# Kernel optimization log

Hardware: AMD Instinct MI355X
Metric: run time of the kernel (lower is better)

## Reference

```python
import jax, jax.numpy as jnp
import numpy as np

EPS = 1e-08


def setup_inputs() -> dict:
    key = jax.random.key(0)
    k1, k2, k3 = jax.random.split(key, 3)
    N = 4000000
    x = jax.random.normal(k1, (N, 3), dtype=jnp.float32)
    x_gt = jax.random.normal(k2, (N, 3), dtype=jnp.float32)
    weights = jax.random.uniform(k3, (N,), dtype=jnp.float32)
    return {"x": x, "x_gt": x_gt, "weights": weights}


def reference(x, x_gt, weights):
    # weights: [N] -> [N, 1]
    w = weights[:, None]
    weight_sum = w.sum() + EPS
    mu = (w * x).sum(axis=0, keepdims=True) / weight_sum        # [1, 3]
    mu_gt = (w * x_gt).sum(axis=0, keepdims=True) / weight_sum  # [1, 3]
    x_c = x - mu
    x_gt_c = x_gt - mu_gt
    sw = jnp.sqrt(w)
    # H = (sqrt(w)*x_c)^T @ (sqrt(w)*x_gt_c)  -> [3, 3]
    H = jnp.einsum('ni,nj->ij', sw * x_c, sw * x_gt_c)
    U, S, Vt = jnp.linalg.svd(H)
    R = U @ Vt  # == U @ V.T with V = Vt.T
    det_R = jnp.linalg.det(R)
    # Reflection fix: R = U @ diag(1,1,d) @ Vt with d = -1 if det < 0
    d = jnp.where(det_R < 0, -1.0, 1.0).astype(R.dtype)
    F = jnp.array([1.0, 1.0, 0.0], dtype=R.dtype) + jnp.array([0.0, 0.0, 1.0], dtype=R.dtype) * d
    R = (U * F[None, :]) @ Vt
    # x_aligned = (R @ x_gt_c^T)^T + mu = x_gt_c @ R^T + mu
    x_aligned = x_gt_c @ R.T + mu
    return jax.lax.stop_gradient(x_aligned)
```

## Files before the change

### kernel.cpp

```cpp
#include <hip/hip_runtime.h>
#include <math.h>

#define BLK 256

__global__ __launch_bounds__(BLK) void wra_reduce(
    const float* __restrict__ x, const float* __restrict__ g,
    const float* __restrict__ w, float* __restrict__ partials,
    int n4, int n, int ntiles)
{
    __shared__ float4 xs[768];
    __shared__ float4 gs[768];
    __shared__ float4 ws[256];

    float a[16];
#pragma unroll
    for (int i = 0; i < 16; ++i) a[i] = 0.f;

    const float4* __restrict__ x4 = (const float4*)x;
    const float4* __restrict__ g4 = (const float4*)g;
    const float4* __restrict__ w4 = (const float4*)w;

    const int tid = threadIdx.x;
    const int totc = 3 * n4;
    const float4 z4 = make_float4(0.f, 0.f, 0.f, 0.f);

    int t = blockIdx.x;
    {
        float4 rx[3], rg[3], rw;
        const int cb = t * 768;
#pragma unroll
        for (int k = 0; k < 3; ++k) {
            int c = cb + tid + 256 * k;
            rx[k] = z4; rg[k] = z4;
            if (c < totc) { rx[k] = x4[c]; rg[k] = g4[c]; }
        }
        int wc = t * 256 + tid;
        rw = (wc < n4) ? w4[wc] : z4;
#pragma unroll
        for (int k = 0; k < 3; ++k) { xs[tid + 256 * k] = rx[k]; gs[tid + 256 * k] = rg[k]; }
        ws[tid] = rw;
    }
    __syncthreads();

    while (t < ntiles) {
        const int tn = t + gridDim.x;
        const bool havenext = (tn < ntiles);
        float4 px[3], pg[3], pw;
        if (havenext) {
            const int cb = tn * 768;
#pragma unroll
            for (int k = 0; k < 3; ++k) {
                int c = cb + tid + 256 * k;
                px[k] = z4; pg[k] = z4;
                if (c < totc) { px[k] = x4[c]; pg[k] = g4[c]; }
            }
            int wc = tn * 256 + tid;
            pw = (wc < n4) ? w4[wc] : z4;
        }

        {
            float4 xa = xs[3 * tid + 0], xb = xs[3 * tid + 1], xc = xs[3 * tid + 2];
            float4 ga = gs[3 * tid + 0], gb = gs[3 * tid + 1], gc = gs[3 * tid + 2];
            float4 wv = ws[tid];

            float pxc[4] = {xa.x, xa.w, xb.z, xc.y};
            float pyc[4] = {xa.y, xb.x, xb.w, xc.z};
            float pzc[4] = {xa.z, xb.y, xc.x, xc.w};
            float qxc[4] = {ga.x, ga.w, gb.z, gc.y};
            float qyc[4] = {ga.y, gb.x, gb.w, gc.z};
            float qzc[4] = {ga.z, gb.y, gc.x, gc.w};
            float wt[4]  = {wv.x, wv.y, wv.z, wv.w};
#pragma unroll
            for (int k = 0; k < 4; ++k) {
                float wk = wt[k];
                float wpx = wk * pxc[k], wpy = wk * pyc[k], wpz = wk * pzc[k];
                a[0] += wk;
                a[1] += wpx;          a[2] += wpy;          a[3] += wpz;
                a[4] += wk * qxc[k];  a[5] += wk * qyc[k];  a[6] += wk * qzc[k];
                a[7]  += wpx * qxc[k]; a[8]  += wpx * qyc[k]; a[9]  += wpx * qzc[k];
                a[10] += wpy * qxc[k]; a[11] += wpy * qyc[k]; a[12] += wpy * qzc[k];
                a[13] += wpz * qxc[k]; a[14] += wpz * qyc[k]; a[15] += wpz * qzc[k];
            }
        }
        __syncthreads();

        if (havenext) {
#pragma unroll
            for (int k = 0; k < 3; ++k) { xs[tid + 256 * k] = px[k]; gs[tid + 256 * k] = pg[k]; }
            ws[tid] = pw;
        }
        __syncthreads();
        t = tn;
    }

    if (blockIdx.x == 0 && tid == 0) {
        for (int r = n4 * 4; r < n; ++r) {
            float wk = w[r];
            float X = x[3 * r], Y = x[3 * r + 1], Z = x[3 * r + 2];
            float Gx = g[3 * r], Gy = g[3 * r + 1], Gz = g[3 * r + 2];
            float wpx = wk * X, wpy = wk * Y, wpz = wk * Z;
            a[0] += wk;
            a[1] += wpx;      a[2] += wpy;      a[3] += wpz;
            a[4] += wk * Gx;  a[5] += wk * Gy;  a[6] += wk * Gz;
            a[7]  += wpx * Gx; a[8]  += wpx * Gy; a[9]  += wpx * Gz;
            a[10] += wpy * Gx; a[11] += wpy * Gy; a[12] += wpy * Gz;
            a[13] += wpz * Gx; a[14] += wpz * Gy; a[15] += wpz * Gz;
        }
    }

#pragma unroll
    for (int i = 0; i < 16; ++i) {
        float v = a[i];
        for (int off = 32; off > 0; off >>= 1) v += __shfl_down(v, off, 64);
        a[i] = v;
    }
    __shared__ float red[4][16];
    int lane = tid & 63;
    int wid  = tid >> 6;
    if (lane == 0) {
#pragma unroll
        for (int i = 0; i < 16; ++i) red[wid][i] = a[i];
    }
    __syncthreads();
    if (tid < 16) {
        float s = red[0][tid] + red[1][tid] + red[2][tid] + red[3][tid];
        partials[blockIdx.x * 16 + tid] = s;
    }
}

__global__ __launch_bounds__(64) void wra_solve(
    const float* __restrict__ partials, int nb, float* __restrict__ rt)
{
    int lane = threadIdx.x;
    double acc[16];
#pragma unroll
    for (int i = 0; i < 16; ++i) acc[i] = 0.0;
    for (int b = lane; b < nb; b += 64) {
#pragma unroll
        for (int i = 0; i < 16; ++i) acc[i] += (double)partials[b * 16 + i];
    }
#pragma unroll
    for (int i = 0; i < 16; ++i) {
        double v = acc[i];
        for (int off = 32; off > 0; off >>= 1) v += __shfl_down(v, off, 64);
        acc[i] = v;
    }
    if (lane != 0) return;

    double Sw = acc[0];
    double Sx[3] = {acc[1], acc[2], acc[3]};
    double Sg[3] = {acc[4], acc[5], acc[6]};
    double Hr[3][3];
    for (int i = 0; i < 3; ++i)
        for (int j = 0; j < 3; ++j) Hr[i][j] = acc[7 + i * 3 + j];

    double W = Sw + 1e-8;
    double mu[3], mg[3];
    for (int i = 0; i < 3; ++i) { mu[i] = Sx[i] / W; mg[i] = Sg[i] / W; }

    double H[3][3];
    for (int i = 0; i < 3; ++i)
        for (int j = 0; j < 3; ++j)
            H[i][j] = Hr[i][j] - mu[i] * Sg[j] - mg[j] * Sx[i] + mu[i] * mg[j] * Sw;

    double A[3][3];
    for (int i = 0; i < 3; ++i)
        for (int j = 0; j < 3; ++j) {
            double s = 0.0;
            for (int k = 0; k < 3; ++k) s += H[k][i] * H[k][j];
            A[i][j] = s;
        }

    double V[3][3] = {{1,0,0},{0,1,0},{0,0,1}};
    const int pr[3] = {0, 0, 1}, qr[3] = {1, 2, 2};
    for (int sweep = 0; sweep < 25; ++sweep) {
        for (int r = 0; r < 3; ++r) {
            int p = pr[r], q = qr[r];
            double apq = A[p][q];
            if (fabs(apq) < 1e-30) continue;
            double tau = (A[q][q] - A[p][p]) / (2.0 * apq);
            double t = (tau >= 0 ? 1.0 : -1.0) / (fabs(tau) + sqrt(1.0 + tau * tau));
            double c = 1.0 / sqrt(1.0 + t * t), s = t * c;
            for (int k = 0; k < 3; ++k) {
                double akp = A[k][p], akq = A[k][q];
                A[k][p] = c * akp - s * akq;
                A[k][q] = s * akp + c * akq;
            }
            for (int k = 0; k < 3; ++k) {
                double apk = A[p][k], aqk = A[q][k];
                A[p][k] = c * apk - s * aqk;
                A[q][k] = s * apk + c * aqk;
            }
            for (int k = 0; k < 3; ++k) {
                double vkp = V[k][p], vkq = V[k][q];
                V[k][p] = c * vkp - s * vkq;
                V[k][q] = s * vkp + c * vkq;
            }
        }
    }
    double lam[3] = {A[0][0], A[1][1], A[2][2]};

    int idx[3] = {0, 1, 2};
    if (lam[idx[0]] < lam[idx[1]]) { int t = idx[0]; idx[0] = idx[1]; idx[1] = t; }
    if (lam[idx[1]] < lam[idx[2]]) { int t = idx[1]; idx[1] = idx[2]; idx[2] = t; }
    if (lam[idx[0]] < lam[idx[1]]) { int t = idx[0]; idx[0] = idx[1]; idx[1] = t; }

    double Vs[3][3], U[3][3];
    for (int k = 0; k < 3; ++k) {
        int c0 = idx[k];
        double l = lam[c0] > 1e-30 ? lam[c0] : 1e-30;
        double inv = 1.0 / sqrt(l);
        for (int i = 0; i < 3; ++i) Vs[i][k] = V[i][c0];
        for (int i = 0; i < 3; ++i) {
            double s = 0.0;
            for (int j = 0; j < 3; ++j) s += H[i][j] * Vs[j][k];
            U[i][k] = s * inv;
        }
    }

    double detH = H[0][0] * (H[1][1] * H[2][2] - H[1][2] * H[2][1])
                - H[0][1] * (H[1][0] * H[2][2] - H[1][2] * H[2][0])
                + H[0][2] * (H[1][0] * H[2][1] - H[1][1] * H[2][0]);
    double d = (detH < 0.0) ? -1.0 : 1.0;

    double R[3][3];
    for (int i = 0; i < 3; ++i)
        for (int j = 0; j < 3; ++j)
            R[i][j] = U[i][0] * Vs[j][0] + U[i][1] * Vs[j][1] + d * U[i][2] * Vs[j][2];

    double tv[3];
    for (int i = 0; i < 3; ++i)
        tv[i] = mu[i] - (R[i][0] * mg[0] + R[i][1] * mg[1] + R[i][2] * mg[2]);

    for (int i = 0; i < 3; ++i)
        for (int j = 0; j < 3; ++j) rt[i * 3 + j] = (float)R[i][j];
    for (int i = 0; i < 3; ++i) rt[9 + i] = (float)tv[i];
}

__global__ __launch_bounds__(BLK) void wra_apply(
    const float* __restrict__ g, const float* __restrict__ rt,
    float* __restrict__ out, int n4, int n, int ntiles)
{
    __shared__ float4 buf[768];

    float R00 = rt[0], R01 = rt[1], R02 = rt[2];
    float R10 = rt[3], R11 = rt[4], R12 = rt[5];
    float R20 = rt[6], R21 = rt[7], R22 = rt[8];
    float t0 = rt[9], t1 = rt[10], t2 = rt[11];

    const float4* __restrict__ g4 = (const float4*)g;
    float4* __restrict__ o4 = (float4*)out;

    const int tid = threadIdx.x;
    const int totc = 3 * n4;

    for (int t = blockIdx.x; t < ntiles; t += gridDim.x) {
        const int cb = t * 768;
#pragma unroll
        for (int k = 0; k < 3; ++k) {
            int c = cb + tid + 256 * k;
            if (c < totc) buf[tid + 256 * k] = g4[c];
        }
        __syncthreads();

        float4 ga = buf[3 * tid + 0], gb = buf[3 * tid + 1], gc = buf[3 * tid + 2];
        float qx0 = ga.x, qy0 = ga.y, qz0 = ga.z;
        float qx1 = ga.w, qy1 = gb.x, qz1 = gb.y;
        float qx2 = gb.z, qy2 = gb.w, qz2 = gc.x;
        float qx3 = gc.y, qy3 = gc.z, qz3 = gc.w;

        float ox0 = R00*qx0 + R01*qy0 + R02*qz0 + t0;
        float oy0 = R10*qx0 + R11*qy0 + R12*qz0 + t1;
        float oz0 = R20*qx0 + R21*qy0 + R22*qz0 + t2;
        float ox1 = R00*qx1 + R01*qy1 + R02*qz1 + t0;
        float oy1 = R10*qx1 + R11*qy1 + R12*qz1 + t1;
        float oz1 = R20*qx1 + R21*qy1 + R22*qz1 + t2;
        float ox2 = R00*qx2 + R01*qy2 + R02*qz2 + t0;
        float oy2 = R10*qx2 + R11*qy2 + R12*qz2 + t1;
        float oz2 = R20*qx2 + R21*qy2 + R22*qz2 + t2;
        float ox3 = R00*qx3 + R01*qy3 + R02*qz3 + t0;
        float oy3 = R10*qx3 + R11*qy3 + R12*qz3 + t1;
        float oz3 = R20*qx3 + R21*qy3 + R22*qz3 + t2;

        buf[3 * tid + 0] = make_float4(ox0, oy0, oz0, ox1);
        buf[3 * tid + 1] = make_float4(oy1, oz1, ox2, oy2);
        buf[3 * tid + 2] = make_float4(oz2, ox3, oy3, oz3);
        __syncthreads();

#pragma unroll
        for (int k = 0; k < 3; ++k) {
            int c = cb + tid + 256 * k;
            if (c < totc) o4[c] = buf[tid + 256 * k];
        }
        __syncthreads();
    }

    int gtid = blockIdx.x * blockDim.x + threadIdx.x;
    int gstr = gridDim.x * blockDim.x;
    for (int r = n4 * 4 + gtid; r < n; r += gstr) {
        float Gx = g[3 * r], Gy = g[3 * r + 1], Gz = g[3 * r + 2];
        out[3 * r + 0] = R00 * Gx + R01 * Gy + R02 * Gz + t0;
        out[3 * r + 1] = R10 * Gx + R11 * Gy + R12 * Gz + t1;
        out[3 * r + 2] = R20 * Gx + R21 * Gy + R22 * Gz + t2;
    }
}

extern "C" void kernel_launch(void* const* d_in, const int* in_sizes, int n_in,
                              void* d_out, int out_size, void* d_ws, size_t ws_size,
                              hipStream_t stream)
{
    const float* x = (const float*)d_in[0];
    const float* g = (const float*)d_in[1];
    const float* w = (const float*)d_in[2];
    float* out = (float*)d_out;

    int n = in_sizes[2];
    int n4 = n / 4;
    int ntiles = (n4 + 255) / 256;
    if (ntiles < 1) ntiles = 1;

    int nbr = 1024;
    int maxnb = (int)((ws_size / sizeof(float) - 12) / 16);
    if (nbr > maxnb) nbr = maxnb;
    if (nbr > ntiles) nbr = ntiles;
    if (nbr < 1) nbr = 1;

    float* partials = (float*)d_ws;
    float* rt = partials + (size_t)nbr * 16;

    wra_reduce<<<nbr, BLK, 0, stream>>>(x, g, w, partials, n4, n, ntiles);
    wra_solve<<<1, 64, 0, stream>>>(partials, nbr, rt);

    int nba = ntiles < 2048 ? ntiles : 2048;
    wra_apply<<<nba, BLK, 0, stream>>>(g, rt, out, n4, n, ntiles);
}
```

Baseline: 56.81 us.

## Launch one block per tile and drop register prefetch in reduce/apply

The reduce and apply kernels now launch one block per tile instead of capping the grid at 1024/2048 blocks. The reduce kernel drops its register double-buffering, loads weights directly to registers instead of shared memory, and adds an unchecked fast path for full tiles. Redundant trailing barriers are removed. The goal is more memory parallelism and less synchronization, at the cost of many more partials for the single-wavefront solve kernel to sum.

New measurement: 78.80 us. 1.39x slower.

```diff
diff --git a/kernel.cpp b/kernel.cpp
--- a/kernel.cpp
+++ b/kernel.cpp
@@ -10,7 +10,6 @@
 {
     __shared__ float4 xs[768];
     __shared__ float4 gs[768];
-    __shared__ float4 ws[256];
 
     float a[16];
 #pragma unroll
@@ -24,73 +23,52 @@
     const int totc = 3 * n4;
     const float4 z4 = make_float4(0.f, 0.f, 0.f, 0.f);
 
-    int t = blockIdx.x;
-    {
-        float4 rx[3], rg[3], rw;
+    for (int t = blockIdx.x; t < ntiles; t += gridDim.x) {
+        if (t != (int)blockIdx.x) __syncthreads();
+
         const int cb = t * 768;
-#pragma unroll
-        for (int k = 0; k < 3; ++k) {
-            int c = cb + tid + 256 * k;
-            rx[k] = z4; rg[k] = z4;
-            if (c < totc) { rx[k] = x4[c]; rg[k] = g4[c]; }
+        if (cb + 768 <= totc) {
+#pragma unroll
+            for (int k = 0; k < 3; ++k) {
+                int c = cb + tid + 256 * k;
+                xs[tid + 256 * k] = x4[c];
+                gs[tid + 256 * k] = g4[c];
+            }
+        } else {
+#pragma unroll
+            for (int k = 0; k < 3; ++k) {
+                int c = cb + tid + 256 * k;
+                float4 xv = z4, gv = z4;
+                if (c < totc) { xv = x4[c]; gv = g4[c]; }
+                xs[tid + 256 * k] = xv;
+                gs[tid + 256 * k] = gv;
+            }
         }
         int wc = t * 256 + tid;
-        rw = (wc < n4) ? w4[wc] : z4;
-#pragma unroll
-        for (int k = 0; k < 3; ++k) { xs[tid + 256 * k] = rx[k]; gs[tid + 256 * k] = rg[k]; }
-        ws[tid] = rw;
-    }
-    __syncthreads();
-
-    while (t < ntiles) {
-        const int tn = t + gridDim.x;
-        const bool havenext = (tn < ntiles);
-        float4 px[3], pg[3], pw;
-        if (havenext) {
-            const int cb = tn * 768;
-#pragma unroll
-            for (int k = 0; k < 3; ++k) {
-                int c = cb + tid + 256 * k;
-                px[k] = z4; pg[k] = z4;
-                if (c < totc) { px[k] = x4[c]; pg[k] = g4[c]; }
-            }
-            int wc = tn * 256 + tid;
-            pw = (wc < n4) ? w4[wc] : z4;
-        }
-
-        {
-            float4 xa = xs[3 * tid + 0], xb = xs[3 * tid + 1], xc = xs[3 * tid + 2];
-            float4 ga = gs[3 * tid + 0], gb = gs[3 * tid + 1], gc = gs[3 * tid + 2];
-            float4 wv = ws[tid];
-
-            float pxc[4] = {xa.x, xa.w, xb.z, xc.y};
-            float pyc[4] = {xa.y, xb.x, xb.w, xc.z};
-            float pzc[4] = {xa.z, xb.y, xc.x, xc.w};
-            float qxc[4] = {ga.x, ga.w, gb.z, gc.y};
-            float qyc[4] = {ga.y, gb.x, gb.w, gc.z};
-            float qzc[4] = {ga.z, gb.y, gc.x, gc.w};
-            float wt[4]  = {wv.x, wv.y, wv.z, wv.w};
-#pragma unroll
-            for (int k = 0; k < 4; ++k) {
-                float wk = wt[k];
-                float wpx = wk * pxc[k], wpy = wk * pyc[k], wpz = wk * pzc[k];
-                a[0] += wk;
-                a[1] += wpx;          a[2] += wpy;          a[3] += wpz;
-                a[4] += wk * qxc[k];  a[5] += wk * qyc[k];  a[6] += wk * qzc[k];
-                a[7]  += wpx * qxc[k]; a[8]  += wpx * qyc[k]; a[9]  += wpx * qzc[k];
-                a[10] += wpy * qxc[k]; a[11] += wpy * qyc[k]; a[12] += wpy * qzc[k];
-                a[13] += wpz * qxc[k]; a[14] += wpz * qyc[k]; a[15] += wpz * qzc[k];
-            }
-        }
+        float4 wv = (wc < n4) ? w4[wc] : z4;
         __syncthreads();
 
-        if (havenext) {
-#pragma unroll
-            for (int k = 0; k < 3; ++k) { xs[tid + 256 * k] = px[k]; gs[tid + 256 * k] = pg[k]; }
-            ws[tid] = pw;
-        }
-        __syncthreads();
-        t = tn;
+        float4 xa = xs[3 * tid + 0], xb = xs[3 * tid + 1], xc = xs[3 * tid + 2];
+        float4 ga = gs[3 * tid + 0], gb = gs[3 * tid + 1], gc = gs[3 * tid + 2];
+
+        float pxc[4] = {xa.x, xa.w, xb.z, xc.y};
+        float pyc[4] = {xa.y, xb.x, xb.w, xc.z};
+        float pzc[4] = {xa.z, xb.y, xc.x, xc.w};
+        float qxc[4] = {ga.x, ga.w, gb.z, gc.y};
+        float qyc[4] = {ga.y, gb.x, gb.w, gc.z};
+        float qzc[4] = {ga.z, gb.y, gc.x, gc.w};
+        float wt[4]  = {wv.x, wv.y, wv.z, wv.w};
+#pragma unroll
+        for (int k = 0; k < 4; ++k) {
+            float wk = wt[k];
+            float wpx = wk * pxc[k], wpy = wk * pyc[k], wpz = wk * pzc[k];
+            a[0] += wk;
+            a[1] += wpx;          a[2] += wpy;          a[3] += wpz;
+            a[4] += wk * qxc[k];  a[5] += wk * qyc[k];  a[6] += wk * qzc[k];
+            a[7]  += wpx * qxc[k]; a[8]  += wpx * qyc[k]; a[9]  += wpx * qzc[k];
+            a[10] += wpy * qxc[k]; a[11] += wpy * qyc[k]; a[12] += wpy * qzc[k];
+            a[13] += wpz * qxc[k]; a[14] += wpz * qyc[k]; a[15] += wpz * qzc[k];
+        }
     }
 
     if (blockIdx.x == 0 && tid == 0) {
@@ -117,6 +95,7 @@
     __shared__ float red[4][16];
     int lane = tid & 63;
     int wid  = tid >> 6;
+    __syncthreads();
     if (lane == 0) {
 #pragma unroll
         for (int i = 0; i < 16; ++i) red[wid][i] = a[i];
@@ -255,6 +234,8 @@
     const int totc = 3 * n4;
 
     for (int t = blockIdx.x; t < ntiles; t += gridDim.x) {
+        if (t != (int)blockIdx.x) __syncthreads();
+
         const int cb = t * 768;
 #pragma unroll
         for (int k = 0; k < 3; ++k) {
@@ -292,7 +273,6 @@
             int c = cb + tid + 256 * k;
             if (c < totc) o4[c] = buf[tid + 256 * k];
         }
-        __syncthreads();
     }
 
     int gtid = blockIdx.x * blockDim.x + threadIdx.x;
@@ -319,10 +299,9 @@
     int ntiles = (n4 + 255) / 256;
     if (ntiles < 1) ntiles = 1;
 
-    int nbr = 1024;
+    int nbr = ntiles;
     int maxnb = (int)((ws_size / sizeof(float) - 12) / 16);
     if (nbr > maxnb) nbr = maxnb;
-    if (nbr > ntiles) nbr = ntiles;
     if (nbr < 1) nbr = 1;
 
     float* partials = (float*)d_ws;
@@ -331,6 +310,5 @@
     wra_reduce<<<nbr, BLK, 0, stream>>>(x, g, w, partials, n4, n, ntiles);
     wra_solve<<<1, 64, 0, stream>>>(partials, nbr, rt);
 
-    int nba = ntiles < 2048 ? ntiles : 2048;
-    wra_apply<<<nba, BLK, 0, stream>>>(g, rt, out, n4, n, ntiles);
+    wra_apply<<<ntiles, BLK, 0, stream>>>(g, rt, out, n4, n, ntiles);
 }
```
